# Optimization experiments

Measured on AMD Instinct MI355X. Metric: run time of the kernel, lower is better.

## Reference

```python
import jax, jax.numpy as jnp
import numpy as np

C = 128        # attention channels (inner_channel)
OUT_C = 256    # bottleneck output channels (in_channel)
NEG = -10000000.0


def conv_bn_relu(x, W, scale, shift):
    """1x1 conv (no bias) + eval-mode BatchNorm folded to scale/shift + ReLU.
    x: [B, Cin, H, W], W: [Cout, Cin]."""
    y = jnp.einsum('oc,bchw->bohw', W, x)
    y = y * scale[None, :, None, None] + shift[None, :, None, None]
    return jax.nn.relu(y)


def setup_inputs() -> dict:
    key = jax.random.key(0)
    ks = jax.random.split(key, 20)
    B, H, W_, K = 4, 128, 128, 1024
    inp = {
        'query_feats': jax.random.normal(ks[0], (B, C, H, W_), jnp.float32),
        'key_feats':   jax.random.normal(ks[1], (B, C, K, 1), jnp.float32),
        'value_feats': jax.random.normal(ks[2], (B, C, K, 1), jnp.float32),
        'key_mask':    jax.random.randint(ks[3], (B, 1, K, 1), 0, 2).astype(bool),
    }
    s = 1.0 / np.sqrt(C)

    def mk(i, cin, cout):
        return (jax.random.normal(ks[i], (cout, cin), jnp.float32) * s,
                jnp.ones((cout,), jnp.float32),
                jnp.zeros((cout,), jnp.float32))

    inp['Wq1'], inp['sq1'], inp['bq1'] = mk(4, C, C)
    inp['Wq2'], inp['sq2'], inp['bq2'] = mk(5, C, C)
    inp['Wk1'], inp['sk1'], inp['bk1'] = mk(6, C, C)
    inp['Wk2'], inp['sk2'], inp['bk2'] = mk(7, C, C)
    inp['Wv'],  inp['sv'],  inp['bv']  = mk(8, C, C)
    inp['Wo'],  inp['so'],  inp['bo']  = mk(9, C, C)
    inp['Wb'],  inp['sb'],  inp['bb']  = mk(10, 2 * C, OUT_C)
    return inp


def reference(query_feats, key_feats, value_feats, key_mask,
              Wq1, sq1, bq1, Wq2, sq2, bq2,
              Wk1, sk1, bk1, Wk2, sk2, bk2,
              Wv, sv, bv, Wo, so, bo, Wb, sb, bb):
    B, _, H, W_ = query_feats.shape
    # projections (2 conv-bn-relu for q/k, 1 for v)
    q = conv_bn_relu(conv_bn_relu(query_feats, Wq1, sq1, bq1), Wq2, sq2, bq2)
    k = conv_bn_relu(conv_bn_relu(key_feats, Wk1, sk1, bk1), Wk2, sk2, bk2)
    v = conv_bn_relu(value_feats, Wv, sv, bv)

    q = q.reshape(B, C, -1).transpose(0, 2, 1)   # [B, HW, C]
    k = k.reshape(B, C, -1)                      # [B, C, K]
    v = v.reshape(B, C, -1).transpose(0, 2, 1)   # [B, K, C]

    sim = jnp.einsum('bqc,bck->bqk', q, k) * (C ** -0.5)   # [B, HW, K]
    m = key_mask.reshape(B, 1, -1).astype(sim.dtype)        # [B, 1, K]
    sim = sim * m + NEG * (1.0 - m)
    attn = jax.nn.softmax(sim, axis=-1)

    ctx = jnp.einsum('bqk,bkc->bqc', attn, v)               # [B, HW, C]
    ctx = ctx.transpose(0, 2, 1).reshape(B, C, H, W_)
    ctx = conv_bn_relu(ctx, Wo, so, bo)                     # out_project

    out = conv_bn_relu(jnp.concatenate([ctx, query_feats], axis=1), Wb, sb, bb)
    return out
```

## Files before the change

kernel.cpp:

```cpp
#include <hip/hip_runtime.h>
#include <hip/hip_bf16.h>

#define B_    4
#define C_    128
#define HW_   16384
#define K_    1024
#define NEG_  (-10000000.0f)
#define SCALE_ 0.08838834764831845f

using bf16 = __hip_bfloat16;
typedef __bf16 b8v __attribute__((ext_vector_type(8)));
typedef __bf16 b4v __attribute__((ext_vector_type(4)));
typedef __bf16 b2v __attribute__((ext_vector_type(2)));
typedef float  f4v __attribute__((ext_vector_type(4)));

__device__ __forceinline__ b8v ldb8(const void* p) { return *(const b8v*)p; }
__device__ __forceinline__ b4v ldb4(const void* p) { return *(const b4v*)p; }

#define XSTRIDE 272

__global__ __launch_bounds__(256) void wprep_kernel(
    const float* __restrict__ Wq1, const float* __restrict__ sq1,
    const float* __restrict__ Wq2, const float* __restrict__ sq2,
    const float* __restrict__ Wo,  const float* __restrict__ so,
    const float* __restrict__ Wb,  const float* __restrict__ sb,
    const float* __restrict__ Wk1, const float* __restrict__ sk1,
    const float* __restrict__ Wk2, const float* __restrict__ sk2,
    const float* __restrict__ Wv,  const float* __restrict__ sv,
    __bf16* __restrict__ Wq1p, __bf16* __restrict__ Wq2p,
    __bf16* __restrict__ Wop,  __bf16* __restrict__ Wbp,
    __bf16* __restrict__ Wk1p, __bf16* __restrict__ Wk2p, __bf16* __restrict__ Wvp)
{
    const int idx = blockIdx.x * 256 + threadIdx.x;
    if (idx < 16384)       { Wq1p[idx] = (__bf16)(Wq1[idx] * sq1[idx >> 7]); }
    else if (idx < 32768)  { const int i = idx - 16384;  Wq2p[i] = (__bf16)(Wq2[i] * sq2[i >> 7]); }
    else if (idx < 49152)  { const int i = idx - 32768;  Wop[i]  = (__bf16)(Wo[i]  * so[i >> 7]); }
    else if (idx < 114688) { const int i = idx - 49152;  Wbp[i]  = (__bf16)(Wb[i]  * sb[i >> 8]); }
    else if (idx < 131072) { const int i = idx - 114688; Wk1p[i] = (__bf16)(Wk1[i] * sk1[i >> 7]); }
    else if (idx < 147456) { const int i = idx - 131072; Wk2p[i] = (__bf16)(Wk2[i] * sk2[i >> 7]); }
    else                   { const int i = idx - 147456; Wvp[i]  = (__bf16)(Wv[i]  * sv[i >> 7]); }
}

__global__ __launch_bounds__(256) void txp_kernel(
    const float* __restrict__ query, const float* __restrict__ key, const float* __restrict__ val,
    bf16* __restrict__ qt, bf16* __restrict__ kT, bf16* __restrict__ vT)
{
    __shared__ float Xs[64 * 129];
    const int seg = blockIdx.x, b = blockIdx.y, t = threadIdx.x;
    const float* src; bf16* dst; int L, p0;
    if (seg < 256)      { src = query; dst = qt; L = HW_; p0 = seg * 64; }
    else if (seg < 272) { src = key;   dst = kT; L = K_;  p0 = (seg - 256) * 64; }
    else                { src = val;   dst = vT; L = K_;  p0 = (seg - 272) * 64; }

    const int pl = t & 63, cg = t >> 6;
#pragma unroll 4
    for (int i = 0; i < 32; ++i) {
        const int c = cg * 32 + i;
        Xs[pl * 129 + c] = src[(size_t)(b * 128 + c) * L + p0 + pl];
    }
    __syncthreads();
#pragma unroll 4
    for (int it = 0; it < 16; ++it) {
        const int p = it * 4 + cg;
        b2v pk;
        pk[0] = (__bf16)Xs[p * 129 + 2 * pl];
        pk[1] = (__bf16)Xs[p * 129 + 2 * pl + 1];
        *(b2v*)(dst + ((size_t)b * L + p0 + p) * 128 + 2 * pl) = pk;
    }
}

__device__ __forceinline__ void proj2_body(
    const bf16* __restrict__ src,
    const __bf16* __restrict__ W1, const float* __restrict__ sh1,
    const __bf16* __restrict__ W2, const float* __restrict__ sh2,
    bf16* __restrict__ dst, char* Xs, __bf16* Ys)
{
    const int t = threadIdx.x, w = t >> 6, lane = t & 63;
    const int pl = lane & 15, quad = lane >> 4;
    const int ob = 32 * w;

    {
        const char* sg = (const char*)src + t * 16;
        char* xl = Xs + (t >> 4) * XSTRIDE + (t & 15) * 16;
#pragma unroll
        for (int i = 0; i < 8; ++i)
            *(float4*)(xl + i * 16 * XSTRIDE) = *(const float4*)(sg + i * 4096);
    }

    b8v W1f[2][4], W2f[2][4];
#pragma unroll
    for (int mt = 0; mt < 2; ++mt)
#pragma unroll
        for (int s = 0; s < 4; ++s) {
            W1f[mt][s] = ldb8(W1 + (ob + mt * 16 + pl) * 128 + s * 32 + quad * 8);
            W2f[mt][s] = ldb8(W2 + (ob + mt * 16 + pl) * 128 + s * 32 + quad * 8);
        }
    __syncthreads();

    f4v acc[2][8];
#pragma unroll
    for (int mt = 0; mt < 2; ++mt)
#pragma unroll
        for (int nt = 0; nt < 8; ++nt) acc[mt][nt] = (f4v){0.f, 0.f, 0.f, 0.f};

#pragma unroll
    for (int s = 0; s < 4; ++s) {
        b8v Bf[8];
#pragma unroll
        for (int nt = 0; nt < 8; ++nt)
            Bf[nt] = ldb8(Xs + (nt * 16 + pl) * XSTRIDE + s * 64 + quad * 16);
#pragma unroll
        for (int mt = 0; mt < 2; ++mt)
#pragma unroll
            for (int nt = 0; nt < 8; ++nt)
                acc[mt][nt] = __builtin_amdgcn_mfma_f32_16x16x32_bf16(W1f[mt][s], Bf[nt], acc[mt][nt], 0, 0, 0);
    }

#pragma unroll
    for (int mt = 0; mt < 2; ++mt) {
        const float4 s4 = *(const float4*)(sh1 + ob + mt * 16 + quad * 4);
        const float shf[4] = {s4.x, s4.y, s4.z, s4.w};
#pragma unroll
        for (int nt = 0; nt < 8; ++nt) {
            b4v y;
#pragma unroll
            for (int r = 0; r < 4; ++r) y[r] = (__bf16)fmaxf(acc[mt][nt][r] + shf[r], 0.f);
            *(b4v*)&Ys[(nt * 16 + pl) * 136 + ob + mt * 16 + quad * 4] = y;
        }
    }
    __syncthreads();

    f4v acc2[2][8];
#pragma unroll
    for (int mt = 0; mt < 2; ++mt)
#pragma unroll
        for (int nt = 0; nt < 8; ++nt) acc2[mt][nt] = (f4v){0.f, 0.f, 0.f, 0.f};

#pragma unroll
    for (int s = 0; s < 4; ++s) {
        b8v Bf[8];
#pragma unroll
        for (int nt = 0; nt < 8; ++nt)
            Bf[nt] = *(const b8v*)&Ys[(nt * 16 + pl) * 136 + s * 32 + quad * 8];
#pragma unroll
        for (int mt = 0; mt < 2; ++mt)
#pragma unroll
            for (int nt = 0; nt < 8; ++nt)
                acc2[mt][nt] = __builtin_amdgcn_mfma_f32_16x16x32_bf16(W2f[mt][s], Bf[nt], acc2[mt][nt], 0, 0, 0);
    }

#pragma unroll
    for (int mt = 0; mt < 2; ++mt) {
        const float4 s4 = *(const float4*)(sh2 + ob + mt * 16 + quad * 4);
        const float shf[4] = {s4.x, s4.y, s4.z, s4.w};
#pragma unroll
        for (int nt = 0; nt < 8; ++nt) {
            b4v y;
#pragma unroll
            for (int r = 0; r < 4; ++r) y[r] = (__bf16)fmaxf(acc2[mt][nt][r] + shf[r], 0.f);
            *(b4v*)(dst + (size_t)(nt * 16 + pl) * 128 + ob + mt * 16 + quad * 4) = y;
        }
    }
}

__global__ __launch_bounds__(256, 2) void proj_kernel(
    const bf16* __restrict__ qt, const bf16* __restrict__ kT, const bf16* __restrict__ vT,
    const __bf16* __restrict__ Wq1p, const float* __restrict__ bq1,
    const __bf16* __restrict__ Wq2p, const float* __restrict__ bq2,
    const __bf16* __restrict__ Wk1p, const float* __restrict__ bk1,
    const __bf16* __restrict__ Wk2p, const float* __restrict__ bk2,
    const __bf16* __restrict__ Wvp,  const float* __restrict__ bv,
    bf16* __restrict__ qbuf, bf16* __restrict__ kbuf, bf16* __restrict__ vbuf)
{
    __shared__ __align__(16) char Xs[128 * XSTRIDE];
    __shared__ __align__(16) __bf16 Ys[128 * 136];
    const int t = threadIdx.x, w = t >> 6, lane = t & 63;
    const int pl = lane & 15, quad = lane >> 4;
    const int b = blockIdx.y;

    if (blockIdx.x < 128) {
        const int n0 = blockIdx.x * 128;
        proj2_body(qt + ((size_t)b * HW_ + n0) * 128, Wq1p, bq1, Wq2p, bq2,
                   qbuf + ((size_t)b * HW_ + n0) * 128, Xs, Ys);
        return;
    }

    const int n0 = (blockIdx.x - 128) * 128;
    proj2_body(kT + ((size_t)b * K_ + n0) * 128, Wk1p, bk1, Wk2p, bk2,
               kbuf + ((size_t)b * K_ + n0) * 128, Xs, Ys);
    __syncthreads();

    {
        const char* sg = (const char*)(vT + ((size_t)b * K_ + n0) * 128) + t * 16;
        char* xl = Xs + (t >> 4) * XSTRIDE + (t & 15) * 16;
#pragma unroll
        for (int i = 0; i < 8; ++i)
            *(float4*)(xl + i * 16 * XSTRIDE) = *(const float4*)(sg + i * 4096);
    }
    const int ob = 32 * w;
    b8v Wf[2][4];
#pragma unroll
    for (int mt = 0; mt < 2; ++mt)
#pragma unroll
        for (int s = 0; s < 4; ++s)
            Wf[mt][s] = ldb8(Wvp + (ob + mt * 16 + pl) * 128 + s * 32 + quad * 8);
    __syncthreads();

    f4v acc[2][8];
#pragma unroll
    for (int mt = 0; mt < 2; ++mt)
#pragma unroll
        for (int nt = 0; nt < 8; ++nt) acc[mt][nt] = (f4v){0.f, 0.f, 0.f, 0.f};

#pragma unroll
    for (int s = 0; s < 4; ++s) {
        b8v Bf[8];
#pragma unroll
        for (int nt = 0; nt < 8; ++nt)
            Bf[nt] = ldb8(Xs + (nt * 16 + pl) * XSTRIDE + s * 64 + quad * 16);
#pragma unroll
        for (int mt = 0; mt < 2; ++mt)
#pragma unroll
            for (int nt = 0; nt < 8; ++nt)
                acc[mt][nt] = __builtin_amdgcn_mfma_f32_16x16x32_bf16(Wf[mt][s], Bf[nt], acc[mt][nt], 0, 0, 0);
    }

    bf16* vb = vbuf + (size_t)b * 128 * K_;
#pragma unroll
    for (int mt = 0; mt < 2; ++mt) {
        const float4 s4 = *(const float4*)(bv + ob + mt * 16 + quad * 4);
        const float shf[4] = {s4.x, s4.y, s4.z, s4.w};
#pragma unroll
        for (int nt = 0; nt < 8; ++nt)
#pragma unroll
            for (int r = 0; r < 4; ++r)
                vb[(size_t)(ob + mt * 16 + quad * 4 + r) * K_ + n0 + nt * 16 + pl]
                    = __float2bfloat16(fmaxf(acc[mt][nt][r] + shf[r], 0.f));
    }
}

#define KSTRIDE 272
#define VSTRIDE 136
__global__ __launch_bounds__(256, 2) void attn_kernel(
    const bf16* __restrict__ qbuf, const bf16* __restrict__ kbuf, const bf16* __restrict__ vbuf,
    const int* __restrict__ mask, bf16* __restrict__ ctxbuf)
{
    __shared__ __align__(16) float bias[K_];
    __shared__ __align__(16) char ktile[64 * KSTRIDE];
    __shared__ __align__(16) char vtile[128 * VSTRIDE];

    const int t    = threadIdx.x;
    const int w    = t >> 6;
    const int lane = t & 63;
    const int m    = lane & 15;
    const int quad = lane >> 4;
    const int q0   = blockIdx.x * 64;
    const int b    = blockIdx.y;

    for (int i = t; i < K_; i += 256)
        bias[i] = (mask[b * K_ + i] != 0) ? 0.f : NEG_;

    b8v qf[4];
    {
        const bf16* qrow = qbuf + ((size_t)b * HW_ + q0 + w * 16 + m) * 128;
#pragma unroll
        for (int s = 0; s < 4; ++s) qf[s] = ldb8(qrow + s * 32 + quad * 8);
    }

    const bf16* kpt = kbuf + (size_t)b * K_ * 128;
    const bf16* vpt = vbuf + (size_t)b * 128 * K_;

    const char* kg = (const char*)kpt + t * 16;
    const char* vg = (const char*)(vpt + (size_t)(t >> 3) * K_) + (t & 7) * 16;
    char* kl = ktile + (t >> 4) * KSTRIDE + (t & 15) * 16;
    char* vl = vtile + (t >> 3) * VSTRIDE + (t & 7) * 16;

    float4 k_r0 = *(const float4*)(kg);
    float4 k_r1 = *(const float4*)(kg + 4096);
    float4 k_r2 = *(const float4*)(kg + 8192);
    float4 k_r3 = *(const float4*)(kg + 12288);
    float4 v_r0 = *(const float4*)(vg);
    float4 v_r1 = *(const float4*)(vg + 65536);
    float4 v_r2 = *(const float4*)(vg + 131072);
    float4 v_r3 = *(const float4*)(vg + 196608);

    f4v acc[8];
#pragma unroll
    for (int i = 0; i < 8; ++i) acc[i] = (f4v){0.f, 0.f, 0.f, 0.f};
    float mrun = -3.0e38f, lrun = 0.f;

    for (int chunk = 0; chunk < 16; ++chunk) {
        const int k0 = chunk * 64;

        *(float4*)(kl)                = k_r0;
        *(float4*)(kl + 16 * KSTRIDE) = k_r1;
        *(float4*)(kl + 32 * KSTRIDE) = k_r2;
        *(float4*)(kl + 48 * KSTRIDE) = k_r3;
        *(float4*)(vl)                = v_r0;
        *(float4*)(vl + 32 * VSTRIDE) = v_r1;
        *(float4*)(vl + 64 * VSTRIDE) = v_r2;
        *(float4*)(vl + 96 * VSTRIDE) = v_r3;
        __syncthreads();

        if (chunk < 15) {
            const char* kgn = kg + (chunk + 1) * 16384;
            const char* vgn = vg + (chunk + 1) * 128;
            k_r0 = *(const float4*)(kgn);
            k_r1 = *(const float4*)(kgn + 4096);
            k_r2 = *(const float4*)(kgn + 8192);
            k_r3 = *(const float4*)(kgn + 12288);
            v_r0 = *(const float4*)(vgn);
            v_r1 = *(const float4*)(vgn + 65536);
            v_r2 = *(const float4*)(vgn + 131072);
            v_r3 = *(const float4*)(vgn + 196608);
        }

        f4v sv[4];
#pragma unroll
        for (int kt = 0; kt < 4; ++kt) {
            f4v a = (f4v){0.f, 0.f, 0.f, 0.f};
            const char* krow = ktile + (kt * 16 + m) * KSTRIDE + quad * 16;
#pragma unroll
            for (int s = 0; s < 4; ++s)
                a = __builtin_amdgcn_mfma_f32_16x16x32_bf16(ldb8(krow + s * 64), qf[s], a, 0, 0, 0);
            const float4 b4 = *(const float4*)&bias[k0 + kt * 16 + quad * 4];
            const float bb4[4] = {b4.x, b4.y, b4.z, b4.w};
#pragma unroll
            for (int r = 0; r < 4; ++r) sv[kt][r] = a[r] * SCALE_ + bb4[r];
        }

        float mloc = sv[0][0];
#pragma unroll
        for (int kt = 0; kt < 4; ++kt)
#pragma unroll
            for (int r = 0; r < 4; ++r) mloc = fmaxf(mloc, sv[kt][r]);
        mloc = fmaxf(mloc, __shfl_xor(mloc, 16, 64));
        mloc = fmaxf(mloc, __shfl_xor(mloc, 32, 64));
        const float mn = fmaxf(mrun, mloc);
        const float alpha = __expf(mrun - mn);
        mrun = mn;

        b4v pk[4];
        float rs = 0.f;
#pragma unroll
        for (int kt = 0; kt < 4; ++kt)
#pragma unroll
            for (int r = 0; r < 4; ++r) {
                const float p = __expf(sv[kt][r] - mn);
                rs += p;
                pk[kt][r] = (__bf16)p;
            }
        rs += __shfl_xor(rs, 16, 64);
        rs += __shfl_xor(rs, 32, 64);
        lrun = lrun * alpha + rs;

        float alr[4];
#pragma unroll
        for (int r = 0; r < 4; ++r) alr[r] = __shfl(alpha, quad * 4 + r, 64);
#pragma unroll
        for (int ct = 0; ct < 8; ++ct)
#pragma unroll
            for (int r = 0; r < 4; ++r) acc[ct][r] *= alr[r];

        const b8v A0 = __builtin_shufflevector(pk[0], pk[1], 0, 1, 2, 3, 4, 5, 6, 7);
        const b8v A1 = __builtin_shufflevector(pk[2], pk[3], 0, 1, 2, 3, 4, 5, 6, 7);
#pragma unroll
        for (int ct = 0; ct < 8; ++ct) {
            const char* vrow = vtile + (ct * 16 + m) * VSTRIDE + quad * 8;
            const b8v B0 = __builtin_shufflevector(ldb4(vrow),      ldb4(vrow + 32), 0, 1, 2, 3, 4, 5, 6, 7);
            const b8v B1 = __builtin_shufflevector(ldb4(vrow + 64), ldb4(vrow + 96), 0, 1, 2, 3, 4, 5, 6, 7);
            acc[ct] = __builtin_amdgcn_mfma_f32_16x16x32_bf16(A0, B0, acc[ct], 0, 0, 0);
            acc[ct] = __builtin_amdgcn_mfma_f32_16x16x32_bf16(A1, B1, acc[ct], 0, 0, 0);
        }
        __syncthreads();
    }

    float inv[4];
#pragma unroll
    for (int r = 0; r < 4; ++r) inv[r] = 1.f / __shfl(lrun, quad * 4 + r, 64);
    bf16* crow = ctxbuf + ((size_t)b * HW_ + q0 + w * 16) * 128;
#pragma unroll
    for (int ct = 0; ct < 8; ++ct)
#pragma unroll
        for (int r = 0; r < 4; ++r)
            crow[(size_t)(quad * 4 + r) * 128 + ct * 16 + m] = __float2bfloat16(acc[ct][r] * inv[r]);
}

__global__ __launch_bounds__(256, 2) void final_kernel(
    const bf16* __restrict__ ctx, const bf16* __restrict__ qt,
    const __bf16* __restrict__ Wop, const float* __restrict__ bo,
    const __bf16* __restrict__ Wbp, const float* __restrict__ bb,
    float* __restrict__ out)
{
    __shared__ __align__(16) char Xs[128 * XSTRIDE];
    __shared__ __align__(16) __bf16 Ys[128 * 136];
    const int t = threadIdx.x, w = t >> 6, lane = t & 63;
    const int pl = lane & 15, quad = lane >> 4;
    const int n0 = blockIdx.x * 128, b = blockIdx.y;
    const int ob = 32 * w;

    char* xl = Xs + (t >> 4) * XSTRIDE + (t & 15) * 16;

    {
        const char* cg = (const char*)(ctx + ((size_t)b * HW_ + n0) * 128) + t * 16;
#pragma unroll
        for (int i = 0; i < 8; ++i)
            *(float4*)(xl + i * 16 * XSTRIDE) = *(const float4*)(cg + i * 4096);
    }

    b8v Wof[2][4];
#pragma unroll
    for (int mt = 0; mt < 2; ++mt)
#pragma unroll
        for (int s = 0; s < 4; ++s)
            Wof[mt][s] = ldb8(Wop + (ob + mt * 16 + pl) * 128 + s * 32 + quad * 8);
    __syncthreads();

    const char* qg = (const char*)(qt + ((size_t)b * HW_ + n0) * 128) + t * 16;
    float4 q_s0 = *(const float4*)(qg);
    float4 q_s1 = *(const float4*)(qg + 4096);
    float4 q_s2 = *(const float4*)(qg + 8192);
    float4 q_s3 = *(const float4*)(qg + 12288);
    float4 q_s4 = *(const float4*)(qg + 16384);
    float4 q_s5 = *(const float4*)(qg + 20480);
    float4 q_s6 = *(const float4*)(qg + 24576);
    float4 q_s7 = *(const float4*)(qg + 28672);

    f4v acc1[2][8];
#pragma unroll
    for (int mt = 0; mt < 2; ++mt)
#pragma unroll
        for (int nt = 0; nt < 8; ++nt) acc1[mt][nt] = (f4v){0.f, 0.f, 0.f, 0.f};

#pragma unroll
    for (int s = 0; s < 4; ++s) {
        b8v Bf[8];
#pragma unroll
        for (int nt = 0; nt < 8; ++nt)
            Bf[nt] = ldb8(Xs + (nt * 16 + pl) * XSTRIDE + s * 64 + quad * 16);
#pragma unroll
        for (int mt = 0; mt < 2; ++mt)
#pragma unroll
            for (int nt = 0; nt < 8; ++nt)
                acc1[mt][nt] = __builtin_amdgcn_mfma_f32_16x16x32_bf16(Wof[mt][s], Bf[nt], acc1[mt][nt], 0, 0, 0);
    }

#pragma unroll
    for (int mt = 0; mt < 2; ++mt) {
        const float4 s4 = *(const float4*)(bo + ob + mt * 16 + quad * 4);
        const float shf[4] = {s4.x, s4.y, s4.z, s4.w};
#pragma unroll
        for (int nt = 0; nt < 8; ++nt) {
            b4v y;
#pragma unroll
            for (int r = 0; r < 4; ++r) y[r] = (__bf16)fmaxf(acc1[mt][nt][r] + shf[r], 0.f);
            *(b4v*)&Ys[(nt * 16 + pl) * 136 + ob + mt * 16 + quad * 4] = y;
        }
    }
    __syncthreads();

    *(float4*)(xl)                 = q_s0;
    *(float4*)(xl + 16 * XSTRIDE)  = q_s1;
    *(float4*)(xl + 32 * XSTRIDE)  = q_s2;
    *(float4*)(xl + 48 * XSTRIDE)  = q_s3;
    *(float4*)(xl + 64 * XSTRIDE)  = q_s4;
    *(float4*)(xl + 80 * XSTRIDE)  = q_s5;
    *(float4*)(xl + 96 * XSTRIDE)  = q_s6;
    *(float4*)(xl + 112 * XSTRIDE) = q_s7;
    __syncthreads();

    f4v acc2[4][8];
#pragma unroll
    for (int mt = 0; mt < 4; ++mt)
#pragma unroll
        for (int nt = 0; nt < 8; ++nt) acc2[mt][nt] = (f4v){0.f, 0.f, 0.f, 0.f};

#pragma unroll
    for (int ks = 0; ks < 8; ++ks) {
        b8v Af[4];
#pragma unroll
        for (int mt = 0; mt < 4; ++mt)
            Af[mt] = ldb8(Wbp + (size_t)(64 * w + mt * 16 + pl) * 256 + ks * 32 + quad * 8);
        b8v Bf[8];
        if (ks < 4) {
#pragma unroll
            for (int nt = 0; nt < 8; ++nt)
                Bf[nt] = *(const b8v*)&Ys[(nt * 16 + pl) * 136 + ks * 32 + quad * 8];
        } else {
#pragma unroll
            for (int nt = 0; nt < 8; ++nt)
                Bf[nt] = ldb8(Xs + (nt * 16 + pl) * XSTRIDE + (ks - 4) * 64 + quad * 16);
        }
#pragma unroll
        for (int mt = 0; mt < 4; ++mt)
#pragma unroll
            for (int nt = 0; nt < 8; ++nt)
                acc2[mt][nt] = __builtin_amdgcn_mfma_f32_16x16x32_bf16(Af[mt], Bf[nt], acc2[mt][nt], 0, 0, 0);
    }

#pragma unroll
    for (int mt = 0; mt < 4; ++mt) {
        const float4 s4 = *(const float4*)(bb + 64 * w + mt * 16 + quad * 4);
        const float shf[4] = {s4.x, s4.y, s4.z, s4.w};
#pragma unroll
        for (int nt = 0; nt < 8; ++nt)
#pragma unroll
            for (int r = 0; r < 4; ++r)
                out[(size_t)(b * 256 + 64 * w + mt * 16 + quad * 4 + r) * HW_ + n0 + nt * 16 + pl]
                    = fmaxf(acc2[mt][nt][r] + shf[r], 0.f);
    }
}

extern "C" void kernel_launch(void* const* d_in, const int* in_sizes, int n_in,
                              void* d_out, int out_size, void* d_ws, size_t ws_size,
                              hipStream_t stream)
{
    const float* query = (const float*)d_in[0];
    const float* key   = (const float*)d_in[1];
    const float* val   = (const float*)d_in[2];
    const int*   mask  = (const int*)  d_in[3];
    const float* Wq1 = (const float*)d_in[4];  const float* sq1 = (const float*)d_in[5];  const float* bq1 = (const float*)d_in[6];
    const float* Wq2 = (const float*)d_in[7];  const float* sq2 = (const float*)d_in[8];  const float* bq2 = (const float*)d_in[9];
    const float* Wk1 = (const float*)d_in[10]; const float* sk1 = (const float*)d_in[11]; const float* bk1 = (const float*)d_in[12];
    const float* Wk2 = (const float*)d_in[13]; const float* sk2 = (const float*)d_in[14]; const float* bk2 = (const float*)d_in[15];
    const float* Wv  = (const float*)d_in[16]; const float* sv  = (const float*)d_in[17]; const float* bv  = (const float*)d_in[18];
    const float* Wo  = (const float*)d_in[19]; const float* so  = (const float*)d_in[20]; const float* bo  = (const float*)d_in[21];
    const float* Wb  = (const float*)d_in[22]; const float* sb  = (const float*)d_in[23]; const float* bb  = (const float*)d_in[24];

    char* ws = (char*)d_ws;
    bf16*   kbuf = (bf16*)(ws);
    bf16*   vbuf = (bf16*)(ws + (1u << 20));
    bf16*   qbuf = (bf16*)(ws + (2u << 20));
    bf16*   ctxb = (bf16*)(ws + (18u << 20));
    bf16*   qt   = (bf16*)(ws + (34u << 20));
    bf16*   kT   = (bf16*)(ws + (50u << 20));
    bf16*   vT   = (bf16*)(ws + (51u << 20));
    char*   wbase = ws + (52u << 20);
    __bf16* Wq1p = (__bf16*)(wbase);
    __bf16* Wq2p = (__bf16*)(wbase + (32u << 10));
    __bf16* Wop  = (__bf16*)(wbase + (64u << 10));
    __bf16* Wbp  = (__bf16*)(wbase + (96u << 10));
    __bf16* Wk1p = (__bf16*)(wbase + (224u << 10));
    __bf16* Wk2p = (__bf16*)(wbase + (256u << 10));
    __bf16* Wvp  = (__bf16*)(wbase + (288u << 10));
    float* outp = (float*)d_out;

    wprep_kernel<<<640, 256, 0, stream>>>(
        Wq1, sq1, Wq2, sq2, Wo, so, Wb, sb, Wk1, sk1, Wk2, sk2, Wv, sv,
        Wq1p, Wq2p, Wop, Wbp, Wk1p, Wk2p, Wvp);
    txp_kernel<<<dim3(288, B_), 256, 0, stream>>>(query, key, val, qt, kT, vT);
    proj_kernel<<<dim3(136, B_), 256, 0, stream>>>(
        qt, kT, vT, Wq1p, bq1, Wq2p, bq2, Wk1p, bk1, Wk2p, bk2, Wvp, bv,
        qbuf, kbuf, vbuf);
    attn_kernel<<<dim3(HW_ / 64, B_), 256, 0, stream>>>(
        qbuf, kbuf, vbuf, mask, ctxb);
    final_kernel<<<dim3(HW_ / 128, B_), 256, 0, stream>>>(
        ctxb, qt, Wop, bo, Wbp, bb, outp);
}
```

Baseline: 247.1 us.

## Fuse query projection, attention and output convs into one kernel per tile

Merges the weight-prep and transpose kernels into a single launch, splits the key/value projection into its own small kernel, and fuses the query projection, flash attention and the output/bottleneck convolutions into one kernel over 128-query tiles. Each wave now handles 32 query rows and reuses each key fragment for two MFMAs. This removes the global round trips for qbuf and ctxbuf and cuts two launches. In exchange the attention grid is halved (128 blocks per batch instead of 256) and register pressure per wave rises, which may reduce occupancy.

```diff
diff --git a/kernel.cpp b/kernel.cpp
--- a/kernel.cpp
+++ b/kernel.cpp
@@ -18,8 +18,11 @@
 __device__ __forceinline__ b4v ldb4(const void* p) { return *(const b4v*)p; }
 
 #define XSTRIDE 272
-
-__global__ __launch_bounds__(256) void wprep_kernel(
+#define KSTRIDE 272
+#define VSTRIDE 136
+
+__global__ __launch_bounds__(256) void prep1_kernel(
+    const float* __restrict__ query, const float* __restrict__ key, const float* __restrict__ val,
     const float* __restrict__ Wq1, const float* __restrict__ sq1,
     const float* __restrict__ Wq2, const float* __restrict__ sq2,
     const float* __restrict__ Wo,  const float* __restrict__ so,
@@ -27,45 +30,48 @@
     const float* __restrict__ Wk1, const float* __restrict__ sk1,
     const float* __restrict__ Wk2, const float* __restrict__ sk2,
     const float* __restrict__ Wv,  const float* __restrict__ sv,
+    bf16* __restrict__ qt, bf16* __restrict__ kT, bf16* __restrict__ vT,
     __bf16* __restrict__ Wq1p, __bf16* __restrict__ Wq2p,
     __bf16* __restrict__ Wop,  __bf16* __restrict__ Wbp,
     __bf16* __restrict__ Wk1p, __bf16* __restrict__ Wk2p, __bf16* __restrict__ Wvp)
 {
-    const int idx = blockIdx.x * 256 + threadIdx.x;
-    if (idx < 16384)       { Wq1p[idx] = (__bf16)(Wq1[idx] * sq1[idx >> 7]); }
-    else if (idx < 32768)  { const int i = idx - 16384;  Wq2p[i] = (__bf16)(Wq2[i] * sq2[i >> 7]); }
-    else if (idx < 49152)  { const int i = idx - 32768;  Wop[i]  = (__bf16)(Wo[i]  * so[i >> 7]); }
-    else if (idx < 114688) { const int i = idx - 49152;  Wbp[i]  = (__bf16)(Wb[i]  * sb[i >> 8]); }
-    else if (idx < 131072) { const int i = idx - 114688; Wk1p[i] = (__bf16)(Wk1[i] * sk1[i >> 7]); }
-    else if (idx < 147456) { const int i = idx - 131072; Wk2p[i] = (__bf16)(Wk2[i] * sk2[i >> 7]); }
-    else                   { const int i = idx - 147456; Wvp[i]  = (__bf16)(Wv[i]  * sv[i >> 7]); }
-}
-
-__global__ __launch_bounds__(256) void txp_kernel(
-    const float* __restrict__ query, const float* __restrict__ key, const float* __restrict__ val,
-    bf16* __restrict__ qt, bf16* __restrict__ kT, bf16* __restrict__ vT)
-{
     __shared__ float Xs[64 * 129];
-    const int seg = blockIdx.x, b = blockIdx.y, t = threadIdx.x;
-    const float* src; bf16* dst; int L, p0;
-    if (seg < 256)      { src = query; dst = qt; L = HW_; p0 = seg * 64; }
-    else if (seg < 272) { src = key;   dst = kT; L = K_;  p0 = (seg - 256) * 64; }
-    else                { src = val;   dst = vT; L = K_;  p0 = (seg - 272) * 64; }
-
-    const int pl = t & 63, cg = t >> 6;
+    const int blk = blockIdx.x, t = threadIdx.x;
+
+    if (blk < 1152) {
+        const float* src; bf16* dst; int L, p0, b;
+        if (blk < 1024) {
+            b = blk >> 8; src = query; dst = qt; L = HW_; p0 = (blk & 255) * 64;
+        } else {
+            const int i = blk - 1024;
+            b = i >> 5; int j = i & 31;
+            if (j < 16) { src = key; dst = kT; } else { src = val; dst = vT; j -= 16; }
+            L = K_; p0 = j * 64;
+        }
+        const int pl = t & 63, cg = t >> 6;
 #pragma unroll 4
-    for (int i = 0; i < 32; ++i) {
-        const int c = cg * 32 + i;
-        Xs[pl * 129 + c] = src[(size_t)(b * 128 + c) * L + p0 + pl];
-    }
-    __syncthreads();
+        for (int i = 0; i < 32; ++i) {
+            const int c = cg * 32 + i;
+            Xs[pl * 129 + c] = src[(size_t)(b * 128 + c) * L + p0 + pl];
+        }
+        __syncthreads();
 #pragma unroll 4
-    for (int it = 0; it < 16; ++it) {
-        const int p = it * 4 + cg;
-        b2v pk;
-        pk[0] = (__bf16)Xs[p * 129 + 2 * pl];
-        pk[1] = (__bf16)Xs[p * 129 + 2 * pl + 1];
-        *(b2v*)(dst + ((size_t)b * L + p0 + p) * 128 + 2 * pl) = pk;
+        for (int it = 0; it < 16; ++it) {
+            const int p = it * 4 + cg;
+            b2v pk;
+            pk[0] = (__bf16)Xs[p * 129 + 2 * pl];
+            pk[1] = (__bf16)Xs[p * 129 + 2 * pl + 1];
+            *(b2v*)(dst + ((size_t)b * L + p0 + p) * 128 + 2 * pl) = pk;
+        }
+    } else {
+        const int idx = (blk - 1152) * 256 + t;
+        if (idx < 16384)       { Wq1p[idx] = (__bf16)(Wq1[idx] * sq1[idx >> 7]); }
+        else if (idx < 32768)  { const int i = idx - 16384;  Wq2p[i] = (__bf16)(Wq2[i] * sq2[i >> 7]); }
+        else if (idx < 49152)  { const int i = idx - 32768;  Wop[i]  = (__bf16)(Wo[i]  * so[i >> 7]); }
+        else if (idx < 114688) { const int i = idx - 49152;  Wbp[i]  = (__bf16)(Wb[i]  * sb[i >> 8]); }
+        else if (idx < 131072) { const int i = idx - 114688; Wk1p[i] = (__bf16)(Wk1[i] * sk1[i >> 7]); }
+        else if (idx < 147456) { const int i = idx - 131072; Wk2p[i] = (__bf16)(Wk2[i] * sk2[i >> 7]); }
+        else                   { const int i = idx - 147456; Wvp[i]  = (__bf16)(Wv[i]  * sv[i >> 7]); }
     }
 }
 
@@ -163,29 +169,20 @@
     }
 }
 
-__global__ __launch_bounds__(256, 2) void proj_kernel(
-    const bf16* __restrict__ qt, const bf16* __restrict__ kT, const bf16* __restrict__ vT,
-    const __bf16* __restrict__ Wq1p, const float* __restrict__ bq1,
-    const __bf16* __restrict__ Wq2p, const float* __restrict__ bq2,
+__global__ __launch_bounds__(256, 2) void kvproj_kernel(
+    const bf16* __restrict__ kT, const bf16* __restrict__ vT,
     const __bf16* __restrict__ Wk1p, const float* __restrict__ bk1,
     const __bf16* __restrict__ Wk2p, const float* __restrict__ bk2,
     const __bf16* __restrict__ Wvp,  const float* __restrict__ bv,
-    bf16* __restrict__ qbuf, bf16* __restrict__ kbuf, bf16* __restrict__ vbuf)
+    bf16* __restrict__ kbuf, bf16* __restrict__ vbuf)
 {
     __shared__ __align__(16) char Xs[128 * XSTRIDE];
     __shared__ __align__(16) __bf16 Ys[128 * 136];
     const int t = threadIdx.x, w = t >> 6, lane = t & 63;
     const int pl = lane & 15, quad = lane >> 4;
     const int b = blockIdx.y;
-
-    if (blockIdx.x < 128) {
-        const int n0 = blockIdx.x * 128;
-        proj2_body(qt + ((size_t)b * HW_ + n0) * 128, Wq1p, bq1, Wq2p, bq2,
-                   qbuf + ((size_t)b * HW_ + n0) * 128, Xs, Ys);
-        return;
-    }
-
-    const int n0 = (blockIdx.x - 128) * 128;
+    const int n0 = blockIdx.x * 128;
+
     proj2_body(kT + ((size_t)b * K_ + n0) * 128, Wk1p, bk1, Wk2p, bk2,
                kbuf + ((size_t)b * K_ + n0) * 128, Xs, Ys);
     __syncthreads();
@@ -239,37 +236,125 @@
     }
 }
 
-#define KSTRIDE 272
-#define VSTRIDE 136
-__global__ __launch_bounds__(256, 2) void attn_kernel(
-    const bf16* __restrict__ qbuf, const bf16* __restrict__ kbuf, const bf16* __restrict__ vbuf,
-    const int* __restrict__ mask, bf16* __restrict__ ctxbuf)
+__global__ __launch_bounds__(256, 2) void mega_kernel(
+    const bf16* __restrict__ qt, const bf16* __restrict__ kbuf, const bf16* __restrict__ vbuf,
+    const int* __restrict__ mask,
+    const __bf16* __restrict__ Wq1p, const float* __restrict__ bq1,
+    const __bf16* __restrict__ Wq2p, const float* __restrict__ bq2,
+    const __bf16* __restrict__ Wop,  const float* __restrict__ bo,
+    const __bf16* __restrict__ Wbp,  const float* __restrict__ bb,
+    float* __restrict__ out)
 {
-    __shared__ __align__(16) float bias[K_];
-    __shared__ __align__(16) char ktile[64 * KSTRIDE];
-    __shared__ __align__(16) char vtile[128 * VSTRIDE];
-
-    const int t    = threadIdx.x;
-    const int w    = t >> 6;
-    const int lane = t & 63;
-    const int m    = lane & 15;
-    const int quad = lane >> 4;
-    const int q0   = blockIdx.x * 64;
-    const int b    = blockIdx.y;
+    __shared__ __align__(16) char RA[128 * XSTRIDE];
+    __shared__ __align__(16) char RB[128 * XSTRIDE];
+
+    const int t = threadIdx.x, w = t >> 6, lane = t & 63;
+    const int pl = lane & 15, quad = lane >> 4;
+    const int n0 = blockIdx.x * 128;
+    const int b  = blockIdx.y;
+    const int ob = 32 * w;
+
+    __bf16* RAh = (__bf16*)RA;
+    __bf16* RBh = (__bf16*)RB;
+    char* xl = RA + (t >> 4) * XSTRIDE + (t & 15) * 16;
+
+    {
+        const char* qg = (const char*)(qt + ((size_t)b * HW_ + n0) * 128) + t * 16;
+#pragma unroll
+        for (int i = 0; i < 8; ++i)
+            *(float4*)(xl + i * 16 * XSTRIDE) = *(const float4*)(qg + i * 4096);
+    }
+    {
+        b8v W1f[2][4], W2f[2][4];
+#pragma unroll
+        for (int mt = 0; mt < 2; ++mt)
+#pragma unroll
+            for (int s = 0; s < 4; ++s) {
+                W1f[mt][s] = ldb8(Wq1p + (ob + mt * 16 + pl) * 128 + s * 32 + quad * 8);
+                W2f[mt][s] = ldb8(Wq2p + (ob + mt * 16 + pl) * 128 + s * 32 + quad * 8);
+            }
+        __syncthreads();
+
+        f4v a1[2][8];
+#pragma unroll
+        for (int mt = 0; mt < 2; ++mt)
+#pragma unroll
+            for (int nt = 0; nt < 8; ++nt) a1[mt][nt] = (f4v){0.f, 0.f, 0.f, 0.f};
+#pragma unroll
+        for (int s = 0; s < 4; ++s) {
+            b8v Bf[8];
+#pragma unroll
+            for (int nt = 0; nt < 8; ++nt)
+                Bf[nt] = ldb8(RA + (nt * 16 + pl) * XSTRIDE + s * 64 + quad * 16);
+#pragma unroll
+            for (int mt = 0; mt < 2; ++mt)
+#pragma unroll
+                for (int nt = 0; nt < 8; ++nt)
+                    a1[mt][nt] = __builtin_amdgcn_mfma_f32_16x16x32_bf16(W1f[mt][s], Bf[nt], a1[mt][nt], 0, 0, 0);
+        }
+#pragma unroll
+        for (int mt = 0; mt < 2; ++mt) {
+            const float4 s4 = *(const float4*)(bq1 + ob + mt * 16 + quad * 4);
+            const float shf[4] = {s4.x, s4.y, s4.z, s4.w};
+#pragma unroll
+            for (int nt = 0; nt < 8; ++nt) {
+                b4v y;
+#pragma unroll
+                for (int r = 0; r < 4; ++r) y[r] = (__bf16)fmaxf(a1[mt][nt][r] + shf[r], 0.f);
+                *(b4v*)&RBh[(nt * 16 + pl) * 136 + ob + mt * 16 + quad * 4] = y;
+            }
+        }
+        __syncthreads();
+
+        f4v a2[2][8];
+#pragma unroll
+        for (int mt = 0; mt < 2; ++mt)
+#pragma unroll
+            for (int nt = 0; nt < 8; ++nt) a2[mt][nt] = (f4v){0.f, 0.f, 0.f, 0.f};
+#pragma unroll
+        for (int s = 0; s < 4; ++s) {
+            b8v Bf[8];
+#pragma unroll
+            for (int nt = 0; nt < 8; ++nt)
+                Bf[nt] = *(const b8v*)&RBh[(nt * 16 + pl) * 136 + s * 32 + quad * 8];
+#pragma unroll
+            for (int mt = 0; mt < 2; ++mt)
+#pragma unroll
+                for (int nt = 0; nt < 8; ++nt)
+                    a2[mt][nt] = __builtin_amdgcn_mfma_f32_16x16x32_bf16(W2f[mt][s], Bf[nt], a2[mt][nt], 0, 0, 0);
+        }
+#pragma unroll
+        for (int mt = 0; mt < 2; ++mt) {
+            const float4 s4 = *(const float4*)(bq2 + ob + mt * 16 + quad * 4);
+            const float shf[4] = {s4.x, s4.y, s4.z, s4.w};
+#pragma unroll
+            for (int nt = 0; nt < 8; ++nt) {
+                b4v y;
+#pragma unroll
+                for (int r = 0; r < 4; ++r) y[r] = (__bf16)fmaxf(a2[mt][nt][r] + shf[r], 0.f);
+                *(b4v*)&RAh[(nt * 16 + pl) * 136 + ob + mt * 16 + quad * 4] = y;
+            }
+        }
+        __syncthreads();
+    }
+
+    b8v qf0[4], qf1[4];
+#pragma unroll
+    for (int s = 0; s < 4; ++s) {
+        qf0[s] = ldb8(RA + (w * 32 + pl) * XSTRIDE + s * 64 + quad * 16);
+        qf1[s] = ldb8(RA + (w * 32 + 16 + pl) * XSTRIDE + s * 64 + quad * 16);
+    }
+    __syncthreads();
+
+    float* bias = (float*)RA;
+    char* ktile = RA + 4096;
+    char* vtile = RB;
 
     for (int i = t; i < K_; i += 256)
         bias[i] = (mask[b * K_ + i] != 0) ? 0.f : NEG_;
 
-    b8v qf[4];
-    {
-        const bf16* qrow = qbuf + ((size_t)b * HW_ + q0 + w * 16 + m) * 128;
-#pragma unroll
-        for (int s = 0; s < 4; ++s) qf[s] = ldb8(qrow + s * 32 + quad * 8);
-    }
-
     const bf16* kpt = kbuf + (size_t)b * K_ * 128;
     const bf16* vpt = vbuf + (size_t)b * 128 * K_;
-
     const char* kg = (const char*)kpt + t * 16;
     const char* vg = (const char*)(vpt + (size_t)(t >> 3) * K_) + (t & 7) * 16;
     char* kl = ktile + (t >> 4) * KSTRIDE + (t & 15) * 16;
@@ -284,10 +369,10 @@
     float4 v_r2 = *(const float4*)(vg + 131072);
     float4 v_r3 = *(const float4*)(vg + 196608);
 
-    f4v acc[8];
-#pragma unroll
-    for (int i = 0; i < 8; ++i) acc[i] = (f4v){0.f, 0.f, 0.f, 0.f};
-    float mrun = -3.0e38f, lrun = 0.f;
+    f4v ac0[8], ac1[8];
+#pragma unroll
+    for (int i = 0; i < 8; ++i) { ac0[i] = (f4v){0.f,0.f,0.f,0.f}; ac1[i] = (f4v){0.f,0.f,0.f,0.f}; }
+    float mrun0 = -3.0e38f, mrun1 = -3.0e38f, lrun0 = 0.f, lrun1 = 0.f;
 
     for (int chunk = 0; chunk < 16; ++chunk) {
         const int k0 = chunk * 64;
@@ -315,98 +400,89 @@
             v_r3 = *(const float4*)(vgn + 196608);
         }
 
-        f4v sv[4];
+        f4v sv0[4], sv1[4];
 #pragma unroll
         for (int kt = 0; kt < 4; ++kt) {
-            f4v a = (f4v){0.f, 0.f, 0.f, 0.f};
-            const char* krow = ktile + (kt * 16 + m) * KSTRIDE + quad * 16;
-#pragma unroll
-            for (int s = 0; s < 4; ++s)
-                a = __builtin_amdgcn_mfma_f32_16x16x32_bf16(ldb8(krow + s * 64), qf[s], a, 0, 0, 0);
+            f4v a0 = (f4v){0.f,0.f,0.f,0.f}, a1 = (f4v){0.f,0.f,0.f,0.f};
+            const char* krow = ktile + (kt * 16 + pl) * KSTRIDE + quad * 16;
+#pragma unroll
+            for (int s = 0; s < 4; ++s) {
+                const b8v kf = ldb8(krow + s * 64);
+                a0 = __builtin_amdgcn_mfma_f32_16x16x32_bf16(kf, qf0[s], a0, 0, 0, 0);
+                a1 = __builtin_amdgcn_mfma_f32_16x16x32_bf16(kf, qf1[s], a1, 0, 0, 0);
+            }
             const float4 b4 = *(const float4*)&bias[k0 + kt * 16 + quad * 4];
             const float bb4[4] = {b4.x, b4.y, b4.z, b4.w};
 #pragma unroll
-            for (int r = 0; r < 4; ++r) sv[kt][r] = a[r] * SCALE_ + bb4[r];
-        }
-
-        float mloc = sv[0][0];
+            for (int r = 0; r < 4; ++r) { sv0[kt][r] = a0[r] * SCALE_ + bb4[r];
+                                          sv1[kt][r] = a1[r] * SCALE_ + bb4[r]; }
+        }
+
+        float ml0 = sv0[0][0], ml1 = sv1[0][0];
 #pragma unroll
         for (int kt = 0; kt < 4; ++kt)
 #pragma unroll
-            for (int r = 0; r < 4; ++r) mloc = fmaxf(mloc, sv[kt][r]);
-        mloc = fmaxf(mloc, __shfl_xor(mloc, 16, 64));
-        mloc = fmaxf(mloc, __shfl_xor(mloc, 32, 64));
-        const float mn = fmaxf(mrun, mloc);
-        const float alpha = __expf(mrun - mn);
-        mrun = mn;
-
-        b4v pk[4];
-        float rs = 0.f;
+            for (int r = 0; r < 4; ++r) { ml0 = fmaxf(ml0, sv0[kt][r]); ml1 = fmaxf(ml1, sv1[kt][r]); }
+        ml0 = fmaxf(ml0, __shfl_xor(ml0, 16, 64)); ml0 = fmaxf(ml0, __shfl_xor(ml0, 32, 64));
+        ml1 = fmaxf(ml1, __shfl_xor(ml1, 16, 64)); ml1 = fmaxf(ml1, __shfl_xor(ml1, 32, 64));
+        const float mn0 = fmaxf(mrun0, ml0), mn1 = fmaxf(mrun1, ml1);
+        const float al0 = __expf(mrun0 - mn0), al1 = __expf(mrun1 - mn1);
+        mrun0 = mn0; mrun1 = mn1;
+
+        b4v pk0[4], pk1[4];
+        float rs0 = 0.f, rs1 = 0.f;
 #pragma unroll
         for (int kt = 0; kt < 4; ++kt)
 #pragma unroll
             for (int r = 0; r < 4; ++r) {
-                const float p = __expf(sv[kt][r] - mn);
-                rs += p;
-                pk[kt][r] = (__bf16)p;
-            }
-        rs += __shfl_xor(rs, 16, 64);
-        rs += __shfl_xor(rs, 32, 64);
-        lrun = lrun * alpha + rs;
-
-        float alr[4];
-#pragma unroll
-        for (int r = 0; r < 4; ++r) alr[r] = __shfl(alpha, quad * 4 + r, 64);
+                const float p0 = __expf(sv0[kt][r] - mn0); rs0 += p0; pk0[kt][r] = (__bf16)p0;
+                const float p1 = __expf(sv1[kt][r] - mn1); rs1 += p1; pk1[kt][r] = (__bf16)p1;
+            }
+        rs0 += __shfl_xor(rs0, 16, 64); rs0 += __shfl_xor(rs0, 32, 64);
+        rs1 += __shfl_xor(rs1, 16, 64); rs1 += __shfl_xor(rs1, 32, 64);
+        lrun0 = lrun0 * al0 + rs0;
+        lrun1 = lrun1 * al1 + rs1;
+
+        float ar0[4], ar1[4];
+#pragma unroll
+        for (int r = 0; r < 4; ++r) { ar0[r] = __shfl(al0, quad * 4 + r, 64);
+                                      ar1[r] = __shfl(al1, quad * 4 + r, 64); }
 #pragma unroll
         for (int ct = 0; ct < 8; ++ct)
 #pragma unroll
-            for (int r = 0; r < 4; ++r) acc[ct][r] *= alr[r];
-
-        const b8v A0 = __builtin_shufflevector(pk[0], pk[1], 0, 1, 2, 3, 4, 5, 6, 7);
-        const b8v A1 = __builtin_shufflevector(pk[2], pk[3], 0, 1, 2, 3, 4, 5, 6, 7);
+            for (int r = 0; r < 4; ++r) { ac0[ct][r] *= ar0[r]; ac1[ct][r] *= ar1[r]; }
+
+        const b8v A00 = __builtin_shufflevector(pk0[0], pk0[1], 0, 1, 2, 3, 4, 5, 6, 7);
+        const b8v A01 = __builtin_shufflevector(pk0[2], pk0[3], 0, 1, 2, 3, 4, 5, 6, 7);
+        const b8v A10 = __builtin_shufflevector(pk1[0], pk1[1], 0, 1, 2, 3, 4, 5, 6, 7);
+        const b8v A11 = __builtin_shufflevector(pk1[2], pk1[3], 0, 1, 2, 3, 4, 5, 6, 7);
 #pragma unroll
         for (int ct = 0; ct < 8; ++ct) {
-            const char* vrow = vtile + (ct * 16 + m) * VSTRIDE + quad * 8;
+            const char* vrow = vtile + (ct * 16 + pl) * VSTRIDE + quad * 8;
             const b8v B0 = __builtin_shufflevector(ldb4(vrow),      ldb4(vrow + 32), 0, 1, 2, 3, 4, 5, 6, 7);
             const b8v B1 = __builtin_shufflevector(ldb4(vrow + 64), ldb4(vrow + 96), 0, 1, 2, 3, 4, 5, 6, 7);
-            acc[ct] = __builtin_amdgcn_mfma_f32_16x16x32_bf16(A0, B0, acc[ct], 0, 0, 0);
-            acc[ct] = __builtin_amdgcn_mfma_f32_16x16x32_bf16(A1, B1, acc[ct], 0, 0, 0);
+            ac0[ct] = __builtin_amdgcn_mfma_f32_16x16x32_bf16(A00, B0, ac0[ct], 0, 0, 0);
+            ac0[ct] = __builtin_amdgcn_mfma_f32_16x16x32_bf16(A01, B1, ac0[ct], 0, 0, 0);
+            ac1[ct] = __builtin_amdgcn_mfma_f32_16x16x32_bf16(A10, B0, ac1[ct], 0, 0, 0);
+            ac1[ct] = __builtin_amdgcn_mfma_f32_16x16x32_bf16(A11, B1, ac1[ct], 0, 0, 0);
         }
         __syncthreads();
     }
 
-    float inv[4];
-#pragma unroll
-    for (int r = 0; r < 4; ++r) inv[r] = 1.f / __shfl(lrun, quad * 4 + r, 64);
-    bf16* crow = ctxbuf + ((size_t)b * HW_ + q0 + w * 16) * 128;
-#pragma unroll
-    for (int ct = 0; ct < 8; ++ct)
-#pragma unroll
-        for (int r = 0; r < 4; ++r)
-            crow[(size_t)(quad * 4 + r) * 128 + ct * 16 + m] = __float2bfloat16(acc[ct][r] * inv[r]);
-}
-
-__global__ __launch_bounds__(256, 2) void final_kernel(
-    const bf16* __restrict__ ctx, const bf16* __restrict__ qt,
-    const __bf16* __restrict__ Wop, const float* __restrict__ bo,
-    const __bf16* __restrict__ Wbp, const float* __restrict__ bb,
-    float* __restrict__ out)
-{
-    __shared__ __align__(16) char Xs[128 * XSTRIDE];
-    __shared__ __align__(16) __bf16 Ys[128 * 136];
-    const int t = threadIdx.x, w = t >> 6, lane = t & 63;
-    const int pl = lane & 15, quad = lane >> 4;
-    const int n0 = blockIdx.x * 128, b = blockIdx.y;
-    const int ob = 32 * w;
-
-    char* xl = Xs + (t >> 4) * XSTRIDE + (t & 15) * 16;
-
     {
-        const char* cg = (const char*)(ctx + ((size_t)b * HW_ + n0) * 128) + t * 16;
-#pragma unroll
-        for (int i = 0; i < 8; ++i)
-            *(float4*)(xl + i * 16 * XSTRIDE) = *(const float4*)(cg + i * 4096);
-    }
+        float inv0[4], inv1[4];
+#pragma unroll
+        for (int r = 0; r < 4; ++r) { inv0[r] = 1.f / __shfl(lrun0, quad * 4 + r, 64);
+                                      inv1[r] = 1.f / __shfl(lrun1, quad * 4 + r, 64); }
+#pragma unroll
+        for (int ct = 0; ct < 8; ++ct)
+#pragma unroll
+            for (int r = 0; r < 4; ++r) {
+                RAh[(w * 32 + quad * 4 + r) * 136 + ct * 16 + pl]      = (__bf16)(ac0[ct][r] * inv0[r]);
+                RAh[(w * 32 + 16 + quad * 4 + r) * 136 + ct * 16 + pl] = (__bf16)(ac1[ct][r] * inv1[r]);
+            }
+    }
+    __syncthreads();
 
     b8v Wof[2][4];
 #pragma unroll
@@ -414,47 +490,46 @@
 #pragma unroll
         for (int s = 0; s < 4; ++s)
             Wof[mt][s] = ldb8(Wop + (ob + mt * 16 + pl) * 128 + s * 32 + quad * 8);
-    __syncthreads();
-
-    const char* qg = (const char*)(qt + ((size_t)b * HW_ + n0) * 128) + t * 16;
-    float4 q_s0 = *(const float4*)(qg);
-    float4 q_s1 = *(const float4*)(qg + 4096);
-    float4 q_s2 = *(const float4*)(qg + 8192);
-    float4 q_s3 = *(const float4*)(qg + 12288);
-    float4 q_s4 = *(const float4*)(qg + 16384);
-    float4 q_s5 = *(const float4*)(qg + 20480);
-    float4 q_s6 = *(const float4*)(qg + 24576);
-    float4 q_s7 = *(const float4*)(qg + 28672);
-
-    f4v acc1[2][8];
-#pragma unroll
-    for (int mt = 0; mt < 2; ++mt)
-#pragma unroll
-        for (int nt = 0; nt < 8; ++nt) acc1[mt][nt] = (f4v){0.f, 0.f, 0.f, 0.f};
-
-#pragma unroll
-    for (int s = 0; s < 4; ++s) {
-        b8v Bf[8];
-#pragma unroll
-        for (int nt = 0; nt < 8; ++nt)
-            Bf[nt] = ldb8(Xs + (nt * 16 + pl) * XSTRIDE + s * 64 + quad * 16);
+
+    const char* qg2 = (const char*)(qt + ((size_t)b * HW_ + n0) * 128) + t * 16;
+    float4 q_s0 = *(const float4*)(qg2);
+    float4 q_s1 = *(const float4*)(qg2 + 4096);
+    float4 q_s2 = *(const float4*)(qg2 + 8192);
+    float4 q_s3 = *(const float4*)(qg2 + 12288);
+    float4 q_s4 = *(const float4*)(qg2 + 16384);
+    float4 q_s5 = *(const float4*)(qg2 + 20480);
+    float4 q_s6 = *(const float4*)(qg2 + 24576);
+    float4 q_s7 = *(const float4*)(qg2 + 28672);
+
+    {
+        f4v f1[2][8];
 #pragma unroll
         for (int mt = 0; mt < 2; ++mt)
 #pragma unroll
+            for (int nt = 0; nt < 8; ++nt) f1[mt][nt] = (f4v){0.f, 0.f, 0.f, 0.f};
+#pragma unroll
+        for (int s = 0; s < 4; ++s) {
+            b8v Bf[8];
+#pragma unroll
             for (int nt = 0; nt < 8; ++nt)
-                acc1[mt][nt] = __builtin_amdgcn_mfma_f32_16x16x32_bf16(Wof[mt][s], Bf[nt], acc1[mt][nt], 0, 0, 0);
-    }
-
-#pragma unroll
-    for (int mt = 0; mt < 2; ++mt) {
-        const float4 s4 = *(const float4*)(bo + ob + mt * 16 + quad * 4);
-        const float shf[4] = {s4.x, s4.y, s4.z, s4.w};
-#pragma unroll
-        for (int nt = 0; nt < 8; ++nt) {
-            b4v y;
-#pragma unroll
-            for (int r = 0; r < 4; ++r) y[r] = (__bf16)fmaxf(acc1[mt][nt][r] + shf[r], 0.f);
-            *(b4v*)&Ys[(nt * 16 + pl) * 136 + ob + mt * 16 + quad * 4] = y;
+                Bf[nt] = ldb8(RA + (nt * 16 + pl) * XSTRIDE + s * 64 + quad * 16);
+#pragma unroll
+            for (int mt = 0; mt < 2; ++mt)
+#pragma unroll
+                for (int nt = 0; nt < 8; ++nt)
+                    f1[mt][nt] = __builtin_amdgcn_mfma_f32_16x16x32_bf16(Wof[mt][s], Bf[nt], f1[mt][nt], 0, 0, 0);
+        }
+#pragma unroll
+        for (int mt = 0; mt < 2; ++mt) {
+            const float4 s4 = *(const float4*)(bo + ob + mt * 16 + quad * 4);
+            const float shf[4] = {s4.x, s4.y, s4.z, s4.w};
+#pragma unroll
+            for (int nt = 0; nt < 8; ++nt) {
+                b4v y;
+#pragma unroll
+                for (int r = 0; r < 4; ++r) y[r] = (__bf16)fmaxf(f1[mt][nt][r] + shf[r], 0.f);
+                *(b4v*)&RBh[(nt * 16 + pl) * 136 + ob + mt * 16 + quad * 4] = y;
+            }
         }
     }
     __syncthreads();
@@ -469,45 +544,45 @@
     *(float4*)(xl + 112 * XSTRIDE) = q_s7;
     __syncthreads();
 
-    f4v acc2[4][8];
-#pragma unroll
-    for (int mt = 0; mt < 4; ++mt)
-#pragma unroll
-        for (int nt = 0; nt < 8; ++nt) acc2[mt][nt] = (f4v){0.f, 0.f, 0.f, 0.f};
-
-#pragma unroll
-    for (int ks = 0; ks < 8; ++ks) {
-        b8v Af[4];
+    {
+        f4v f2[4][8];
 #pragma unroll
         for (int mt = 0; mt < 4; ++mt)
-            Af[mt] = ldb8(Wbp + (size_t)(64 * w + mt * 16 + pl) * 256 + ks * 32 + quad * 8);
-        b8v Bf[8];
-        if (ks < 4) {
+#pragma unroll
+            for (int nt = 0; nt < 8; ++nt) f2[mt][nt] = (f4v){0.f, 0.f, 0.f, 0.f};
+#pragma unroll
+        for (int ks = 0; ks < 8; ++ks) {
+            b8v Af[4];
+#pragma unroll
+            for (int mt = 0; mt < 4; ++mt)
+                Af[mt] = ldb8(Wbp + (size_t)(64 * w + mt * 16 + pl) * 256 + ks * 32 + quad * 8);
+            b8v Bf[8];
+            if (ks < 4) {
+#pragma unroll
+                for (int nt = 0; nt < 8; ++nt)
+                    Bf[nt] = *(const b8v*)&RBh[(nt * 16 + pl) * 136 + ks * 32 + quad * 8];
+            } else {
+#pragma unroll
+                for (int nt = 0; nt < 8; ++nt)
+                    Bf[nt] = ldb8(RA + (nt * 16 + pl) * XSTRIDE + (ks - 4) * 64 + quad * 16);
+            }
+#pragma unroll
+            for (int mt = 0; mt < 4; ++mt)
+#pragma unroll
+                for (int nt = 0; nt < 8; ++nt)
+                    f2[mt][nt] = __builtin_amdgcn_mfma_f32_16x16x32_bf16(Af[mt], Bf[nt], f2[mt][nt], 0, 0, 0);
+        }
+#pragma unroll
+        for (int mt = 0; mt < 4; ++mt) {
+            const float4 s4 = *(const float4*)(bb + 64 * w + mt * 16 + quad * 4);
+            const float shf[4] = {s4.x, s4.y, s4.z, s4.w};
 #pragma unroll
             for (int nt = 0; nt < 8; ++nt)
-                Bf[nt] = *(const b8v*)&Ys[(nt * 16 + pl) * 136 + ks * 32 + quad * 8];
-        } else {
-#pragma unroll
-            for (int nt = 0; nt < 8; ++nt)
-                Bf[nt] = ldb8(Xs + (nt * 16 + pl) * XSTRIDE + (ks - 4) * 64 + quad * 16);
-        }
-#pragma unroll
-        for (int mt = 0; mt < 4; ++mt)
-#pragma unroll
-            for (int nt = 0; nt < 8; ++nt)
-                acc2[mt][nt] = __builtin_amdgcn_mfma_f32_16x16x32_bf16(Af[mt], Bf[nt], acc2[mt][nt], 0, 0, 0);
-    }
-
-#pragma unroll
-    for (int mt = 0; mt < 4; ++mt) {
-        const float4 s4 = *(const float4*)(bb + 64 * w + mt * 16 + quad * 4);
-        const float shf[4] = {s4.x, s4.y, s4.z, s4.w};
-#pragma unroll
-        for (int nt = 0; nt < 8; ++nt)
-#pragma unroll
-            for (int r = 0; r < 4; ++r)
-                out[(size_t)(b * 256 + 64 * w + mt * 16 + quad * 4 + r) * HW_ + n0 + nt * 16 + pl]
-                    = fmaxf(acc2[mt][nt][r] + shf[r], 0.f);
+#pragma unroll
+                for (int r = 0; r < 4; ++r)
+                    out[(size_t)(b * 256 + 64 * w + mt * 16 + quad * 4 + r) * HW_ + n0 + nt * 16 + pl]
+                        = fmaxf(f2[mt][nt][r] + shf[r], 0.f);
+        }
     }
 }
 
@@ -528,14 +603,12 @@
     const float* Wb  = (const float*)d_in[22]; const float* sb  = (const float*)d_in[23]; const float* bb  = (const float*)d_in[24];
 
     char* ws = (char*)d_ws;
-    bf16*   kbuf = (bf16*)(ws);
-    bf16*   vbuf = (bf16*)(ws + (1u << 20));
-    bf16*   qbuf = (bf16*)(ws + (2u << 20));
-    bf16*   ctxb = (bf16*)(ws + (18u << 20));
-    bf16*   qt   = (bf16*)(ws + (34u << 20));
-    bf16*   kT   = (bf16*)(ws + (50u << 20));
-    bf16*   vT   = (bf16*)(ws + (51u << 20));
-    char*   wbase = ws + (52u << 20);
+    bf16*   qt   = (bf16*)(ws);
+    bf16*   kT   = (bf16*)(ws + (16u << 20));
+    bf16*   vT   = (bf16*)(ws + (17u << 20));
+    bf16*   kbuf = (bf16*)(ws + (18u << 20));
+    bf16*   vbuf = (bf16*)(ws + (19u << 20));
+    char*   wbase = ws + (20u << 20);
     __bf16* Wq1p = (__bf16*)(wbase);
     __bf16* Wq2p = (__bf16*)(wbase + (32u << 10));
     __bf16* Wop  = (__bf16*)(wbase + (64u << 10));
@@ -545,15 +618,13 @@
     __bf16* Wvp  = (__bf16*)(wbase + (288u << 10));
     float* outp = (float*)d_out;
 
-    wprep_kernel<<<640, 256, 0, stream>>>(
+    prep1_kernel<<<1792, 256, 0, stream>>>(
+        query, key, val,
         Wq1, sq1, Wq2, sq2, Wo, so, Wb, sb, Wk1, sk1, Wk2, sk2, Wv, sv,
-        Wq1p, Wq2p, Wop, Wbp, Wk1p, Wk2p, Wvp);
-    txp_kernel<<<dim3(288, B_), 256, 0, stream>>>(query, key, val, qt, kT, vT);
-    proj_kernel<<<dim3(136, B_), 256, 0, stream>>>(
-        qt, kT, vT, Wq1p, bq1, Wq2p, bq2, Wk1p, bk1, Wk2p, bk2, Wvp, bv,
-        qbuf, kbuf, vbuf);
-    attn_kernel<<<dim3(HW_ / 64, B_), 256, 0, stream>>>(
-        qbuf, kbuf, vbuf, mask, ctxb);
-    final_kernel<<<dim3(HW_ / 128, B_), 256, 0, stream>>>(
-        ctxb, qt, Wop, bo, Wbp, bb, outp);
+        qt, kT, vT, Wq1p, Wq2p, Wop, Wbp, Wk1p, Wk2p, Wvp);
+    kvproj_kernel<<<dim3(8, B_), 256, 0, stream>>>(
+        kT, vT, Wk1p, bk1, Wk2p, bk2, Wvp, bv, kbuf, vbuf);
+    mega_kernel<<<dim3(HW_ / 128, B_), 256, 0, stream>>>(
+        qt, kbuf, vbuf, mask,
+        Wq1p, bq1, Wq2p, bq2, Wop, bo, Wbp, bb, outp);
 }
```

Result: faster. 225.3 us (-8.8%).
